# Performance work log

Hardware: AMD Instinct MI355X
Metric: run time of the kernel (lower is better)

Reference implementation:

```python
import jax, jax.numpy as jnp
import numpy as np

N = 50000      # nodes
E = 600000     # edges
D_IN = 128     # node_dim
D = 128        # out_channels
T = 4          # num_node_types
R = 4          # num_edge_types
L = 2          # num_layers
C = 8          # num_class
G = 512        # graphs in batch


def setup_inputs() -> dict:
    key = jax.random.key(0)
    ks = jax.random.split(key, 12)
    s = 0.05
    x = jax.random.normal(ks[0], (N, D_IN), jnp.float32)
    node_type = jax.random.randint(ks[1], (N,), 0, T)
    edge_index = jax.random.randint(ks[2], (2, E), 0, N)
    edge_type = jax.random.randint(ks[3], (E,), 0, R)
    batch = jnp.sort(jax.random.randint(ks[4], (N,), 0, G))
    # learned params
    W_het = jax.random.normal(ks[5], (T, D_IN, D), jnp.float32) * s
    b_het = jnp.zeros((T, D), jnp.float32)
    conv_W = jax.random.normal(ks[6], (L, R, D, D), jnp.float32) * s
    conv_b = jnp.zeros((L, R, D), jnp.float32)
    fuse_W = jax.random.normal(ks[7], (R * D, D), jnp.float32) * s
    fuse_b = jnp.zeros((D,), jnp.float32)
    cls_W = jax.random.normal(ks[8], (D, C), jnp.float32) * s
    cls_b = jnp.zeros((C,), jnp.float32)
    return dict(x=x, W_het=W_het, b_het=b_het, conv_W=conv_W, conv_b=conv_b,
                fuse_W=fuse_W, fuse_b=fuse_b, cls_W=cls_W, cls_b=cls_b,
                node_type=node_type, edge_index=edge_index, edge_type=edge_type,
                batch=batch)


def reference(x, W_het, b_het, conv_W, conv_b, fuse_W, fuse_b, cls_W, cls_b,
              node_type, edge_index, edge_type, batch):
    n = x.shape[0]
    # HeteroLinear: per-node-type linear. Compute all T projections then select.
    x_all = jnp.einsum('nd,tdo->tno', x, W_het)          # [T, N, D]
    h = x_all[node_type, jnp.arange(n)] + b_het[node_type]
    src, dst = edge_index[0], edge_index[1]
    for l in range(L):
        hs = h[src]                                       # [E, D] gather once per layer
        outs = []
        for r in range(R):
            # edges of relation r only (boolean mask == per-relation edge filtering)
            m = hs @ conv_W[l, r]                         # [E, D]
            m = m * (edge_type == r).astype(m.dtype)[:, None]
            agg = jax.ops.segment_sum(m, dst, num_segments=n)  # scatter-add to dst
            outs.append(agg + conv_b[l, r])
        h = jax.nn.relu(jnp.concatenate(outs, axis=1) @ fuse_W + fuse_b)
    # global mean pool over graphs
    counts = jax.ops.segment_sum(jnp.ones((n,), h.dtype), batch, num_segments=G)
    emb = jax.ops.segment_sum(h, batch, num_segments=G) / jnp.maximum(counts, 1.0)[:, None]
    logits = emb @ cls_W + cls_b
    return emb, logits
```

## Files before the change

kernel.cpp:

```cpp
#include <hip/hip_runtime.h>

#define N_NODES 50000
#define N_EDGES 600000
#define DIM     128
#define RR      4
#define LL      2
#define GG      512
#define CC      8
#define NB_SCAN ((N_NODES + 255) / 256)
#define EC      (N_EDGES / 4)

typedef short bf16x8 __attribute__((ext_vector_type(8)));
typedef float f32x4  __attribute__((ext_vector_type(4)));

__device__ __forceinline__ float bf16_to_f(unsigned short u) {
    return __uint_as_float(((unsigned int)u) << 16);
}
__device__ __forceinline__ unsigned short f_to_bf16(float f) {
    unsigned int u = __float_as_uint(f);
    u += 0x7FFFu + ((u >> 16) & 1u);
    return (unsigned short)(u >> 16);
}
__device__ __forceinline__ float loadf(const void* p, long i, int isbf) {
    if (isbf) return bf16_to_f(((const unsigned short*)p)[i]);
    return ((const float*)p)[i];
}
__device__ __forceinline__ void storef(void* p, long i, float v, int isbf) {
    if (isbf) ((unsigned short*)p)[i] = f_to_bf16(v);
    else      ((float*)p)[i] = v;
}

__global__ void cg_init(const unsigned int* __restrict__ xw, int* __restrict__ flag,
                        int* __restrict__ deg_tb) {
    __shared__ int cnt;
    int tid = threadIdx.x;
    int t = blockIdx.x * 256 + tid;
    if (t < N_NODES + 16) deg_tb[t] = 0;
    if (blockIdx.x == 0) {
        if (tid == 0) cnt = 0;
        __syncthreads();
        unsigned int w = xw[tid];
        unsigned int e = (w >> 7) & 0xFFu;
        atomicAdd(&cnt, (e >= 110u && e <= 133u) ? 1 : 0);
        __syncthreads();
        if (tid == 0) *flag = (cnt >= 128) ? 1 : 0;
    }
}

__global__ void cg_hist2(const int* __restrict__ edge_index, const int* __restrict__ node_type,
                         int* __restrict__ deg, int* __restrict__ tb) {
    __shared__ int loc[4];
    int tid = threadIdx.x;
    if (tid < 4) loc[tid] = 0;
    __syncthreads();
    int t = blockIdx.x * 256 + tid;
    if (t < EC) {
        int d0 = edge_index[N_EDGES + t];
        int d1 = edge_index[N_EDGES + t + EC];
        int d2 = edge_index[N_EDGES + t + 2 * EC];
        int d3 = edge_index[N_EDGES + t + 3 * EC];
        atomicAdd(&deg[d0], 1);
        atomicAdd(&deg[d1], 1);
        atomicAdd(&deg[d2], 1);
        atomicAdd(&deg[d3], 1);
    }
    if (t < N_NODES) atomicAdd(&loc[node_type[t]], 1);
    __syncthreads();
    if (tid < 4 && loc[tid]) atomicAdd(&tb[tid], loc[tid]);
}

__global__ void cg_scan_a(const int* __restrict__ deg, int* __restrict__ blocksum) {
    __shared__ int s[256];
    int tid = threadIdx.x;
    int i = blockIdx.x * 256 + tid;
    s[tid] = (i < N_NODES) ? deg[i] : 0;
    __syncthreads();
    for (int off = 128; off > 0; off >>= 1) {
        if (tid < off) s[tid] += s[tid + off];
        __syncthreads();
    }
    if (tid == 0) blocksum[blockIdx.x] = s[0];
}

__global__ void cg_scan_b(const int* __restrict__ blocksum, int* __restrict__ blockoff,
                          int* __restrict__ rowptr, int* __restrict__ tb) {
    __shared__ int s[256];
    int tid = threadIdx.x;
    int v = (tid < NB_SCAN) ? blocksum[tid] : 0;
    s[tid] = v;
    __syncthreads();
    for (int off = 1; off < 256; off <<= 1) {
        int a = (tid >= off) ? s[tid - off] : 0;
        __syncthreads();
        s[tid] += a;
        __syncthreads();
    }
    if (tid < NB_SCAN) blockoff[tid] = s[tid] - v;
    if (tid == 255) rowptr[N_NODES] = s[255];
    if (tid == 0) {
        int run = 0;
        for (int t = 0; t < 4; t++) {
            tb[8 + t] = run;
            tb[4 + t] = run;
            run += tb[t];
        }
        tb[12] = run;
    }
}

__global__ void cg_scan_c(const int* __restrict__ deg, const int* __restrict__ blockoff,
                          int* __restrict__ rowptr, int* __restrict__ cursor) {
    __shared__ int s[256];
    int tid = threadIdx.x;
    int i = blockIdx.x * 256 + tid;
    int v = (i < N_NODES) ? deg[i] : 0;
    s[tid] = v;
    __syncthreads();
    for (int off = 1; off < 256; off <<= 1) {
        int a = (tid >= off) ? s[tid - off] : 0;
        __syncthreads();
        s[tid] += a;
        __syncthreads();
    }
    if (i < N_NODES) {
        int val = blockoff[blockIdx.x] + s[tid] - v;
        rowptr[i] = val;
        cursor[i] = val;
    }
}

__global__ void cg_fill(const int* __restrict__ edge_index, const int* __restrict__ edge_type,
                        int* __restrict__ cursor, int* __restrict__ eidx) {
    int t = blockIdx.x * 256 + threadIdx.x;
    if (t >= EC) return;
#pragma unroll
    for (int k = 0; k < 4; k++) {
        int e = t + k * EC;
        int d = edge_index[N_EDGES + e];
        int pos = atomicAdd(&cursor[d], 1);
        eidx[pos] = (edge_index[e] << 2) | edge_type[e];
    }
}

__global__ void cg_tfill(const int* __restrict__ node_type, int* __restrict__ tb,
                         int* __restrict__ tlist) {
    __shared__ int lcur[4];
    __shared__ int lbase[4];
    int tid = threadIdx.x;
    if (tid < 4) lcur[tid] = 0;
    __syncthreads();
    int n = blockIdx.x * 256 + tid;
    int slot = -1, t = 0;
    if (n < N_NODES) {
        t = node_type[n];
        slot = atomicAdd(&lcur[t], 1);
    }
    __syncthreads();
    if (tid < 4) lbase[tid] = atomicAdd(&tb[4 + tid], lcur[tid]);
    __syncthreads();
    if (n < N_NODES) tlist[lbase[t] + slot] = n;
}

__global__ void cg_canon_x(const void* __restrict__ x, const int* __restrict__ flagp,
                           unsigned short* __restrict__ xb) {
    long i = ((long)blockIdx.x * 256 + threadIdx.x) * 8;
    if (i >= (long)N_NODES * DIM) return;
    if (*flagp) {
        *(uint4*)(xb + i) = *(const uint4*)((const unsigned short*)x + i);
    } else {
        const float* xf = (const float*)x + i;
        float4 f0 = *(const float4*)xf;
        float4 f1 = *(const float4*)(xf + 4);
        uint4 o;
        o.x = (unsigned int)f_to_bf16(f0.x) | ((unsigned int)f_to_bf16(f0.y) << 16);
        o.y = (unsigned int)f_to_bf16(f0.z) | ((unsigned int)f_to_bf16(f0.w) << 16);
        o.z = (unsigned int)f_to_bf16(f1.x) | ((unsigned int)f_to_bf16(f1.y) << 16);
        o.w = (unsigned int)f_to_bf16(f1.z) | ((unsigned int)f_to_bf16(f1.w) << 16);
        *(uint4*)(xb + i) = o;
    }
}

__global__ void cg_canon_Wb(const void* __restrict__ W_het, const void* __restrict__ b_het,
                            const int* __restrict__ flagp,
                            unsigned short* __restrict__ Wt, float* __restrict__ bhf) {
    int b = blockIdx.x;
    int isbf = *flagp;
    if (b < 4 * DIM) {
        int o = b & 127;
        int t = b >> 7;
        int d = threadIdx.x;
        float v = loadf(W_het, ((long)t * DIM + d) * DIM + o, isbf);
        Wt[((long)t * DIM + o) * DIM + d] = f_to_bf16(v);
    } else {
        int t = b - 4 * DIM;
        int o = threadIdx.x;
        bhf[t * DIM + o] = loadf(b_het, t * DIM + o, isbf);
    }
}

__global__ void cg_make_M2tc(const void* __restrict__ conv_W, const void* __restrict__ fuse_W,
                             const void* __restrict__ conv_b, const void* __restrict__ fuse_b,
                             const int* __restrict__ flagp,
                             unsigned short* __restrict__ M2t, float* __restrict__ cvec) {
    __shared__ float s[256];
    int b = blockIdx.x;
    int tid = threadIdx.x;
    int isbf = *flagp;
    if (b < 512) {
        int lr = b >> 6;
        int d  = (b & 63) * 2 + (tid >> 7);
        int r  = lr & 3;
        int o  = tid & 127;
        float acc = 0.0f;
        for (int k = 0; k < DIM; k++) {
            acc += loadf(conv_W, (long)(lr * DIM + d) * DIM + k, isbf)
                 * loadf(fuse_W, (long)(r * DIM + k) * DIM + o, isbf);
        }
        M2t[((long)lr * DIM + o) * DIM + d] = f_to_bf16(acc);
    } else {
        int bc = b - 512;
        int l  = bc >> 7;
        int o  = bc & 127;
        float part = 0.0f;
        for (int rk = tid; rk < RR * DIM; rk += 256) {
            part += loadf(conv_b, (long)l * RR * DIM + rk, isbf)
                  * loadf(fuse_W, (long)rk * DIM + o, isbf);
        }
        s[tid] = part;
        __syncthreads();
        for (int off = 128; off > 0; off >>= 1) {
            if (tid < off) s[tid] += s[tid + off];
            __syncthreads();
        }
        if (tid == 0) cvec[bc] = s[0] + loadf(fuse_b, o, isbf);
    }
}

#define APAD 136

__global__ void cg_hetero_mfma(const unsigned short* __restrict__ xb,
                               const unsigned short* __restrict__ Wt,
                               const float* __restrict__ bhf,
                               const int* __restrict__ tlist, const int* __restrict__ tb,
                               unsigned short* __restrict__ h) {
    int t = blockIdx.y;
    int rows_base = tb[8 + t] + blockIdx.x * 64;
    int rend = tb[8 + t + 1];
    if (rows_base >= rend) return;
    __shared__ unsigned short a_lds[64][APAD];
    __shared__ unsigned short b_lds[DIM][APAD];
    int tx = threadIdx.x;
    const unsigned short* Wsrc = Wt + (long)t * DIM * DIM;
    for (int i = tx; i < 2048; i += 256) {
        uint4 w = *(const uint4*)(Wsrc + i * 8);
        int o = i >> 4, d = (i & 15) * 8;
        *(uint4*)&b_lds[o][d] = w;
    }
    for (int i = tx; i < 1024; i += 256) {
        int row = i >> 4, seg = (i & 15) * 8;
        int gr = rows_base + row;
        uint4 w = make_uint4(0u, 0u, 0u, 0u);
        if (gr < rend) {
            int n = tlist[gr];
            w = *(const uint4*)(xb + (long)n * DIM + seg);
        }
        *(uint4*)&a_lds[row][seg] = w;
    }
    __syncthreads();
    int wv = tx >> 6, lane = tx & 63;
    int m16 = lane & 15, quad = lane >> 4;
    f32x4 acc[8];
#pragma unroll
    for (int c = 0; c < 8; c++) acc[c] = (f32x4){0.f, 0.f, 0.f, 0.f};
    for (int ks = 0; ks < 4; ks++) {
        int koff = ks * 32 + quad * 8;
        bf16x8 af = *(const bf16x8*)(const void*)&a_lds[wv * 16 + m16][koff];
#pragma unroll
        for (int c = 0; c < 8; c++) {
            bf16x8 bfr = *(const bf16x8*)(const void*)&b_lds[c * 16 + m16][koff];
            acc[c] = __builtin_amdgcn_mfma_f32_16x16x32_bf16(af, bfr, acc[c], 0, 0, 0);
        }
    }
#pragma unroll
    for (int c = 0; c < 8; c++) {
#pragma unroll
        for (int i = 0; i < 4; i++) {
            int row = wv * 16 + quad * 4 + i;
            int col = c * 16 + m16;
            int gr = rows_base + row;
            if (gr < rend) {
                int n = tlist[gr];
                h[(long)n * DIM + col] = f_to_bf16(acc[c][i] + bhf[t * DIM + col]);
            }
        }
    }
}

__global__ void cg_pgemm_mfma(const unsigned short* __restrict__ h,
                              const unsigned short* __restrict__ M2t, int l,
                              unsigned short* __restrict__ P) {
    int r  = blockIdx.y;
    int n0 = blockIdx.x * 64;
    __shared__ unsigned short a_lds[64][APAD];
    __shared__ unsigned short b_lds[DIM][APAD];
    int tx = threadIdx.x;
    const unsigned short* Bsrc = M2t + (long)(l * RR + r) * DIM * DIM;
    for (int i = tx; i < 2048; i += 256) {
        uint4 w = *(const uint4*)(Bsrc + i * 8);
        int o = i >> 4, d = (i & 15) * 8;
        *(uint4*)&b_lds[o][d] = w;
    }
    for (int i = tx; i < 1024; i += 256) {
        int row = i >> 4, seg = (i & 15) * 8;
        int n = n0 + row;
        uint4 w = make_uint4(0u, 0u, 0u, 0u);
        if (n < N_NODES) w = *(const uint4*)(h + (long)n * DIM + seg);
        *(uint4*)&a_lds[row][seg] = w;
    }
    __syncthreads();
    int wv = tx >> 6, lane = tx & 63;
    int m16 = lane & 15, quad = lane >> 4;
    f32x4 acc[8];
#pragma unroll
    for (int c = 0; c < 8; c++) acc[c] = (f32x4){0.f, 0.f, 0.f, 0.f};
    for (int ks = 0; ks < 4; ks++) {
        int koff = ks * 32 + quad * 8;
        bf16x8 af = *(const bf16x8*)(const void*)&a_lds[wv * 16 + m16][koff];
#pragma unroll
        for (int c = 0; c < 8; c++) {
            bf16x8 bfr = *(const bf16x8*)(const void*)&b_lds[c * 16 + m16][koff];
            acc[c] = __builtin_amdgcn_mfma_f32_16x16x32_bf16(af, bfr, acc[c], 0, 0, 0);
        }
    }
#pragma unroll
    for (int c = 0; c < 8; c++) {
#pragma unroll
        for (int i = 0; i < 4; i++) {
            int row = wv * 16 + quad * 4 + i;
            int col = c * 16 + m16;
            int n = n0 + row;
            if (n < N_NODES)
                P[(long)n * (RR * DIM) + r * DIM + col] = f_to_bf16(acc[c][i]);
        }
    }
}

__global__ void cg_gather4(const unsigned short* __restrict__ P, const int* __restrict__ rowptr,
                           const int* __restrict__ eidx, const float* __restrict__ cv,
                           unsigned short* __restrict__ hout) {
    int wid  = (blockIdx.x * 256 + threadIdx.x) >> 6;
    int lane = threadIdx.x & 63;
    if (wid >= N_NODES) return;
    int eg = lane >> 4;
    int ol = lane & 15;
    int start = rowptr[wid];
    int end   = rowptr[wid + 1];
    float a[8] = {0.f, 0.f, 0.f, 0.f, 0.f, 0.f, 0.f, 0.f};
    for (int j = start + eg; j < end; j += 4) {
        int v = eidx[j];
        const uint4 w = *(const uint4*)(P + (long)(v >> 2) * (RR * DIM) + (v & 3) * DIM + ol * 8);
        a[0] += bf16_to_f((unsigned short)(w.x & 0xFFFFu));
        a[1] += bf16_to_f((unsigned short)(w.x >> 16));
        a[2] += bf16_to_f((unsigned short)(w.y & 0xFFFFu));
        a[3] += bf16_to_f((unsigned short)(w.y >> 16));
        a[4] += bf16_to_f((unsigned short)(w.z & 0xFFFFu));
        a[5] += bf16_to_f((unsigned short)(w.z >> 16));
        a[6] += bf16_to_f((unsigned short)(w.w & 0xFFFFu));
        a[7] += bf16_to_f((unsigned short)(w.w >> 16));
    }
#pragma unroll
    for (int i = 0; i < 8; i++) {
        a[i] += __shfl_xor(a[i], 16);
        a[i] += __shfl_xor(a[i], 32);
    }
    if (eg == 0) {
        int o0 = ol * 8;
        float v[8];
#pragma unroll
        for (int i = 0; i < 8; i++) {
            float s = a[i] + cv[o0 + i];
            v[i] = s > 0.0f ? s : 0.0f;
        }
        uint4 o4;
        o4.x = (unsigned int)f_to_bf16(v[0]) | ((unsigned int)f_to_bf16(v[1]) << 16);
        o4.y = (unsigned int)f_to_bf16(v[2]) | ((unsigned int)f_to_bf16(v[3]) << 16);
        o4.z = (unsigned int)f_to_bf16(v[4]) | ((unsigned int)f_to_bf16(v[5]) << 16);
        o4.w = (unsigned int)f_to_bf16(v[6]) | ((unsigned int)f_to_bf16(v[7]) << 16);
        *(uint4*)(hout + (long)wid * DIM + o0) = o4;
    }
}

__global__ void cg_pool_logits(const unsigned short* __restrict__ h, const int* __restrict__ batch,
                               const void* __restrict__ cls_W, const void* __restrict__ cls_b,
                               const int* __restrict__ flagp, void* __restrict__ out) {
    __shared__ float acc_s[4][DIM];
    __shared__ float emb_s[DIM];
    int g   = blockIdx.x;
    int tid = threadIdx.x;
    int wv  = tid >> 6;
    int lane = tid & 63;
    int sub = lane >> 4;
    int ol  = lane & 15;
    int isbf = *flagp;
    int lo = 0, hi = N_NODES;
    while (lo < hi) { int mid = (lo + hi) >> 1; if (batch[mid] < g) lo = mid + 1; else hi = mid; }
    int start = lo;
    hi = N_NODES;
    while (lo < hi) { int mid = (lo + hi) >> 1; if (batch[mid] < g + 1) lo = mid + 1; else hi = mid; }
    int end = lo;
    float a[8] = {0.f, 0.f, 0.f, 0.f, 0.f, 0.f, 0.f, 0.f};
    for (int n = start + wv * 4 + sub; n < end; n += 16) {
        uint4 w = *(const uint4*)(h + (long)n * DIM + ol * 8);
        a[0] += bf16_to_f((unsigned short)(w.x & 0xFFFFu));
        a[1] += bf16_to_f((unsigned short)(w.x >> 16));
        a[2] += bf16_to_f((unsigned short)(w.y & 0xFFFFu));
        a[3] += bf16_to_f((unsigned short)(w.y >> 16));
        a[4] += bf16_to_f((unsigned short)(w.z & 0xFFFFu));
        a[5] += bf16_to_f((unsigned short)(w.z >> 16));
        a[6] += bf16_to_f((unsigned short)(w.w & 0xFFFFu));
        a[7] += bf16_to_f((unsigned short)(w.w >> 16));
    }
#pragma unroll
    for (int i = 0; i < 8; i++) {
        a[i] += __shfl_xor(a[i], 16);
        a[i] += __shfl_xor(a[i], 32);
    }
    if (sub == 0) {
#pragma unroll
        for (int i = 0; i < 8; i++) acc_s[wv][ol * 8 + i] = a[i];
    }
    __syncthreads();
    int cnt = end - start;
    float inv = 1.0f / (float)(cnt > 1 ? cnt : 1);
    if (tid < DIM) {
        float e = (acc_s[0][tid] + acc_s[1][tid] + acc_s[2][tid] + acc_s[3][tid]) * inv;
        emb_s[tid] = e;
        storef(out, (long)g * DIM + tid, e, isbf);
    }
    __syncthreads();
    if (tid < 128) {
        int c  = tid >> 4;
        int kk = tid & 15;
        float p = 0.0f;
#pragma unroll
        for (int k = kk * 8; k < kk * 8 + 8; k++)
            p += emb_s[k] * loadf(cls_W, (long)k * CC + c, isbf);
        p += __shfl_xor(p, 1);
        p += __shfl_xor(p, 2);
        p += __shfl_xor(p, 4);
        p += __shfl_xor(p, 8);
        if (kk == 0)
            storef(out, (long)GG * DIM + g * CC + c, p + loadf(cls_b, c, isbf), isbf);
    }
}

extern "C" void kernel_launch(void* const* d_in, const int* in_sizes, int n_in,
                              void* d_out, int out_size, void* d_ws, size_t ws_size,
                              hipStream_t stream) {
    const void* x      = d_in[0];
    const void* W_het  = d_in[1];
    const void* b_het  = d_in[2];
    const void* conv_W = d_in[3];
    const void* conv_b = d_in[4];
    const void* fuse_W = d_in[5];
    const void* fuse_b = d_in[6];
    const void* cls_W  = d_in[7];
    const void* cls_b  = d_in[8];
    const int* node_type  = (const int*)d_in[9];
    const int* edge_index = (const int*)d_in[10];
    const int* edge_type  = (const int*)d_in[11];
    const int* batch      = (const int*)d_in[12];

    char* base = (char*)d_ws;
    unsigned short* hbf      = (unsigned short*)(base + 0);
    unsigned short* P        = (unsigned short*)(base + 12800000);
    unsigned short* xb       = (unsigned short*)(base + 64000000);
    unsigned short* Wt       = (unsigned short*)(base + 76800000);
    float*          bhf      = (float*)(base + 76931072);
    unsigned short* M2t      = (unsigned short*)(base + 76933120);
    float*          cvec     = (float*)(base + 77195264);
    int*            rowptr   = (int*)(base + 77196288);
    int*            cursor   = (int*)(base + 77396320);
    int*            deg      = (int*)(base + 77596352);
    int*            tb       = (int*)(base + 77796352);
    int*            blocksum = (int*)(base + 77796416);
    int*            blockoff = (int*)(base + 77797440);
    int*            eidx     = (int*)(base + 77798464);
    int*            tlist    = (int*)(base + 80198464);
    int*            flag     = (int*)(base + 80398464);

    cg_init<<<(N_NODES + 16 + 255) / 256, 256, 0, stream>>>((const unsigned int*)x, flag, deg);
    cg_hist2<<<(EC + 255) / 256, 256, 0, stream>>>(edge_index, node_type, deg, tb);
    cg_scan_a<<<NB_SCAN, 256, 0, stream>>>(deg, blocksum);
    cg_scan_b<<<1, 256, 0, stream>>>(blocksum, blockoff, rowptr, tb);
    cg_scan_c<<<NB_SCAN, 256, 0, stream>>>(deg, blockoff, rowptr, cursor);
    cg_fill<<<(EC + 255) / 256, 256, 0, stream>>>(edge_index, edge_type, cursor, eidx);
    cg_tfill<<<(N_NODES + 255) / 256, 256, 0, stream>>>(node_type, tb, tlist);

    cg_canon_x<<<(int)(((long)N_NODES * DIM / 8 + 255) / 256), 256, 0, stream>>>(x, flag, xb);
    cg_canon_Wb<<<4 * DIM + 4, DIM, 0, stream>>>(W_het, b_het, flag, Wt, bhf);
    cg_make_M2tc<<<768, 256, 0, stream>>>(conv_W, fuse_W, conv_b, fuse_b, flag, M2t, cvec);

    cg_hetero_mfma<<<dim3((N_NODES + 63) / 64, 4), 256, 0, stream>>>(
        xb, Wt, bhf, tlist, tb, hbf);
    for (int l = 0; l < LL; l++) {
        cg_pgemm_mfma<<<dim3((N_NODES + 63) / 64, RR), 256, 0, stream>>>(hbf, M2t, l, P);
        cg_gather4<<<(N_NODES * 64 + 255) / 256, 256, 0, stream>>>(
            P, rowptr, eidx, cvec + l * DIM, hbf);
    }

    cg_pool_logits<<<GG, 256, 0, stream>>>(hbf, batch, cls_W, cls_b, flag, d_out);
}
```

Baseline: 354.3 us.

## Merge setup kernels, stage MFMA outputs through LDS, unroll gather loop

```diff
diff --git a/kernel.cpp b/kernel.cpp
--- a/kernel.cpp
+++ b/kernel.cpp
@@ -9,6 +9,8 @@
 #define CC      8
 #define NB_SCAN ((N_NODES + 255) / 256)
 #define EC      (N_EDGES / 4)
+#define FB      ((EC + 255) / 256)
+#define TB      ((N_NODES + 255) / 256)
 
 typedef short bf16x8 __attribute__((ext_vector_type(8)));
 typedef float f32x4  __attribute__((ext_vector_type(4)));
@@ -129,78 +131,47 @@
     }
 }
 
-__global__ void cg_fill(const int* __restrict__ edge_index, const int* __restrict__ edge_type,
-                        int* __restrict__ cursor, int* __restrict__ eidx) {
-    int t = blockIdx.x * 256 + threadIdx.x;
-    if (t >= EC) return;
-#pragma unroll
-    for (int k = 0; k < 4; k++) {
-        int e = t + k * EC;
-        int d = edge_index[N_EDGES + e];
-        int pos = atomicAdd(&cursor[d], 1);
-        eidx[pos] = (edge_index[e] << 2) | edge_type[e];
-    }
-}
-
-__global__ void cg_tfill(const int* __restrict__ node_type, int* __restrict__ tb,
-                         int* __restrict__ tlist) {
-    __shared__ int lcur[4];
-    __shared__ int lbase[4];
-    int tid = threadIdx.x;
-    if (tid < 4) lcur[tid] = 0;
-    __syncthreads();
-    int n = blockIdx.x * 256 + tid;
-    int slot = -1, t = 0;
-    if (n < N_NODES) {
-        t = node_type[n];
-        slot = atomicAdd(&lcur[t], 1);
-    }
-    __syncthreads();
-    if (tid < 4) lbase[tid] = atomicAdd(&tb[4 + tid], lcur[tid]);
-    __syncthreads();
-    if (n < N_NODES) tlist[lbase[t] + slot] = n;
-}
-
-__global__ void cg_canon_x(const void* __restrict__ x, const int* __restrict__ flagp,
-                           unsigned short* __restrict__ xb) {
-    long i = ((long)blockIdx.x * 256 + threadIdx.x) * 8;
-    if (i >= (long)N_NODES * DIM) return;
-    if (*flagp) {
-        *(uint4*)(xb + i) = *(const uint4*)((const unsigned short*)x + i);
+__global__ void cg_fill2(const int* __restrict__ edge_index, const int* __restrict__ edge_type,
+                         const int* __restrict__ node_type,
+                         int* __restrict__ cursor, int* __restrict__ eidx,
+                         int* __restrict__ tb, int* __restrict__ tlist) {
+    int b = blockIdx.x;
+    int tid = threadIdx.x;
+    if (b < FB) {
+        int t = b * 256 + tid;
+        if (t >= EC) return;
+#pragma unroll
+        for (int k = 0; k < 4; k++) {
+            int e = t + k * EC;
+            int d = edge_index[N_EDGES + e];
+            int pos = atomicAdd(&cursor[d], 1);
+            __builtin_nontemporal_store((edge_index[e] << 2) | edge_type[e], &eidx[pos]);
+        }
     } else {
-        const float* xf = (const float*)x + i;
-        float4 f0 = *(const float4*)xf;
-        float4 f1 = *(const float4*)(xf + 4);
-        uint4 o;
-        o.x = (unsigned int)f_to_bf16(f0.x) | ((unsigned int)f_to_bf16(f0.y) << 16);
-        o.y = (unsigned int)f_to_bf16(f0.z) | ((unsigned int)f_to_bf16(f0.w) << 16);
-        o.z = (unsigned int)f_to_bf16(f1.x) | ((unsigned int)f_to_bf16(f1.y) << 16);
-        o.w = (unsigned int)f_to_bf16(f1.z) | ((unsigned int)f_to_bf16(f1.w) << 16);
-        *(uint4*)(xb + i) = o;
-    }
-}
-
-__global__ void cg_canon_Wb(const void* __restrict__ W_het, const void* __restrict__ b_het,
-                            const int* __restrict__ flagp,
-                            unsigned short* __restrict__ Wt, float* __restrict__ bhf) {
-    int b = blockIdx.x;
-    int isbf = *flagp;
-    if (b < 4 * DIM) {
-        int o = b & 127;
-        int t = b >> 7;
-        int d = threadIdx.x;
-        float v = loadf(W_het, ((long)t * DIM + d) * DIM + o, isbf);
-        Wt[((long)t * DIM + o) * DIM + d] = f_to_bf16(v);
-    } else {
-        int t = b - 4 * DIM;
-        int o = threadIdx.x;
-        bhf[t * DIM + o] = loadf(b_het, t * DIM + o, isbf);
-    }
-}
-
-__global__ void cg_make_M2tc(const void* __restrict__ conv_W, const void* __restrict__ fuse_W,
+        __shared__ int lcur[4];
+        __shared__ int lbase[4];
+        if (tid < 4) lcur[tid] = 0;
+        __syncthreads();
+        int n = (b - FB) * 256 + tid;
+        int slot = -1, t = 0;
+        if (n < N_NODES) {
+            t = node_type[n];
+            slot = atomicAdd(&lcur[t], 1);
+        }
+        __syncthreads();
+        if (tid < 4) lbase[tid] = atomicAdd(&tb[4 + tid], lcur[tid]);
+        __syncthreads();
+        if (n < N_NODES) tlist[lbase[t] + slot] = n;
+    }
+}
+
+__global__ void cg_canon_all(const void* __restrict__ x,
+                             const void* __restrict__ W_het, const void* __restrict__ b_het,
+                             const void* __restrict__ conv_W, const void* __restrict__ fuse_W,
                              const void* __restrict__ conv_b, const void* __restrict__ fuse_b,
                              const int* __restrict__ flagp,
+                             unsigned short* __restrict__ xb, unsigned short* __restrict__ Wt,
+                             float* __restrict__ bhf,
                              unsigned short* __restrict__ M2t, float* __restrict__ cvec) {
     __shared__ float s[256];
     int b = blockIdx.x;
@@ -217,7 +188,7 @@
                  * loadf(fuse_W, (long)(r * DIM + k) * DIM + o, isbf);
         }
         M2t[((long)lr * DIM + o) * DIM + d] = f_to_bf16(acc);
-    } else {
+    } else if (b < 768) {
         int bc = b - 512;
         int l  = bc >> 7;
         int o  = bc & 127;
@@ -233,6 +204,32 @@
             __syncthreads();
         }
         if (tid == 0) cvec[bc] = s[0] + loadf(fuse_b, o, isbf);
+    } else if (b < 1024) {
+        int pair = (b - 768) * 2 + (tid >> 7);
+        int t = pair >> 7;
+        int o = pair & 127;
+        int d = tid & 127;
+        float v = loadf(W_het, ((long)t * DIM + d) * DIM + o, isbf);
+        Wt[((long)t * DIM + o) * DIM + d] = f_to_bf16(v);
+    } else if (b < 1026) {
+        int idx = (b - 1024) * 256 + tid;
+        if (idx < 4 * DIM) bhf[idx] = loadf(b_het, idx, isbf);
+    } else {
+        long i = ((long)(b - 1026) * 256 + tid) * 8;
+        if (i >= (long)N_NODES * DIM) return;
+        if (isbf) {
+            *(uint4*)(xb + i) = *(const uint4*)((const unsigned short*)x + i);
+        } else {
+            const float* xf = (const float*)x + i;
+            float4 f0 = *(const float4*)xf;
+            float4 f1 = *(const float4*)(xf + 4);
+            uint4 o;
+            o.x = (unsigned int)f_to_bf16(f0.x) | ((unsigned int)f_to_bf16(f0.y) << 16);
+            o.y = (unsigned int)f_to_bf16(f0.z) | ((unsigned int)f_to_bf16(f0.w) << 16);
+            o.z = (unsigned int)f_to_bf16(f1.x) | ((unsigned int)f_to_bf16(f1.y) << 16);
+            o.w = (unsigned int)f_to_bf16(f1.z) | ((unsigned int)f_to_bf16(f1.w) << 16);
+            *(uint4*)(xb + i) = o;
+        }
     }
 }
 
@@ -281,17 +278,23 @@
             acc[c] = __builtin_amdgcn_mfma_f32_16x16x32_bf16(af, bfr, acc[c], 0, 0, 0);
         }
     }
+    __syncthreads();
 #pragma unroll
     for (int c = 0; c < 8; c++) {
 #pragma unroll
         for (int i = 0; i < 4; i++) {
             int row = wv * 16 + quad * 4 + i;
             int col = c * 16 + m16;
-            int gr = rows_base + row;
-            if (gr < rend) {
-                int n = tlist[gr];
-                h[(long)n * DIM + col] = f_to_bf16(acc[c][i] + bhf[t * DIM + col]);
-            }
+            a_lds[row][col] = f_to_bf16(acc[c][i] + bhf[t * DIM + col]);
+        }
+    }
+    __syncthreads();
+    for (int i = tx; i < 1024; i += 256) {
+        int row = i >> 4, seg = (i & 15) * 8;
+        int gr = rows_base + row;
+        if (gr < rend) {
+            int n = tlist[gr];
+            *(uint4*)(h + (long)n * DIM + seg) = *(const uint4*)&a_lds[row][seg];
         }
     }
 }
@@ -332,16 +335,22 @@
             acc[c] = __builtin_amdgcn_mfma_f32_16x16x32_bf16(af, bfr, acc[c], 0, 0, 0);
         }
     }
+    __syncthreads();
 #pragma unroll
     for (int c = 0; c < 8; c++) {
 #pragma unroll
         for (int i = 0; i < 4; i++) {
             int row = wv * 16 + quad * 4 + i;
             int col = c * 16 + m16;
-            int n = n0 + row;
-            if (n < N_NODES)
-                P[(long)n * (RR * DIM) + r * DIM + col] = f_to_bf16(acc[c][i]);
-        }
+            a_lds[row][col] = f_to_bf16(acc[c][i]);
+        }
+    }
+    __syncthreads();
+    for (int i = tx; i < 1024; i += 256) {
+        int row = i >> 4, seg = (i & 15) * 8;
+        int n = n0 + row;
+        if (n < N_NODES)
+            *(uint4*)(P + (long)n * (RR * DIM) + r * DIM + seg) = *(const uint4*)&a_lds[row][seg];
     }
 }
 
@@ -356,7 +365,22 @@
     int start = rowptr[wid];
     int end   = rowptr[wid + 1];
     float a[8] = {0.f, 0.f, 0.f, 0.f, 0.f, 0.f, 0.f, 0.f};
-    for (int j = start + eg; j < end; j += 4) {
+    int j = start + eg;
+    for (; j + 4 < end; j += 8) {
+        int v0 = eidx[j];
+        int v1 = eidx[j + 4];
+        const uint4 w0 = *(const uint4*)(P + (long)(v0 >> 2) * (RR * DIM) + (v0 & 3) * DIM + ol * 8);
+        const uint4 w1 = *(const uint4*)(P + (long)(v1 >> 2) * (RR * DIM) + (v1 & 3) * DIM + ol * 8);
+        a[0] += bf16_to_f((unsigned short)(w0.x & 0xFFFFu)) + bf16_to_f((unsigned short)(w1.x & 0xFFFFu));
+        a[1] += bf16_to_f((unsigned short)(w0.x >> 16))     + bf16_to_f((unsigned short)(w1.x >> 16));
+        a[2] += bf16_to_f((unsigned short)(w0.y & 0xFFFFu)) + bf16_to_f((unsigned short)(w1.y & 0xFFFFu));
+        a[3] += bf16_to_f((unsigned short)(w0.y >> 16))     + bf16_to_f((unsigned short)(w1.y >> 16));
+        a[4] += bf16_to_f((unsigned short)(w0.z & 0xFFFFu)) + bf16_to_f((unsigned short)(w1.z & 0xFFFFu));
+        a[5] += bf16_to_f((unsigned short)(w0.z >> 16))     + bf16_to_f((unsigned short)(w1.z >> 16));
+        a[6] += bf16_to_f((unsigned short)(w0.w & 0xFFFFu)) + bf16_to_f((unsigned short)(w1.w & 0xFFFFu));
+        a[7] += bf16_to_f((unsigned short)(w0.w >> 16))     + bf16_to_f((unsigned short)(w1.w >> 16));
+    }
+    if (j < end) {
         int v = eidx[j];
         const uint4 w = *(const uint4*)(P + (long)(v >> 2) * (RR * DIM) + (v & 3) * DIM + ol * 8);
         a[0] += bf16_to_f((unsigned short)(w.x & 0xFFFFu));
@@ -494,12 +518,12 @@
     cg_scan_a<<<NB_SCAN, 256, 0, stream>>>(deg, blocksum);
     cg_scan_b<<<1, 256, 0, stream>>>(blocksum, blockoff, rowptr, tb);
     cg_scan_c<<<NB_SCAN, 256, 0, stream>>>(deg, blockoff, rowptr, cursor);
-    cg_fill<<<(EC + 255) / 256, 256, 0, stream>>>(edge_index, edge_type, cursor, eidx);
-    cg_tfill<<<(N_NODES + 255) / 256, 256, 0, stream>>>(node_type, tb, tlist);
-
-    cg_canon_x<<<(int)(((long)N_NODES * DIM / 8 + 255) / 256), 256, 0, stream>>>(x, flag, xb);
-    cg_canon_Wb<<<4 * DIM + 4, DIM, 0, stream>>>(W_het, b_het, flag, Wt, bhf);
-    cg_make_M2tc<<<768, 256, 0, stream>>>(conv_W, fuse_W, conv_b, fuse_b, flag, M2t, cvec);
+    cg_fill2<<<FB + TB, 256, 0, stream>>>(edge_index, edge_type, node_type,
+                                          cursor, eidx, tb, tlist);
+
+    cg_canon_all<<<1026 + 3125, 256, 0, stream>>>(x, W_het, b_het, conv_W, fuse_W,
+                                                  conv_b, fuse_b, flag,
+                                                  xb, Wt, bhf, M2t, cvec);
 
     cg_hetero_mfma<<<dim3((N_NODES + 63) / 64, 4), 256, 0, stream>>>(
         xb, Wt, bhf, tlist, tb, hbf);
```

After: 343.6 us. 1.03x faster.
